# Performance work log

Hardware: AMD Instinct MI355X
Metric: run time of the kernel (lower is better)

## Reference

```python
import jax, jax.numpy as jnp
import numpy as np

B, S, IN, D, H, L, M = 8, 1024, 256, 512, 8, 2, 64
DK = D // H
FF = 4 * D
EPS = 1e-5


def setup_inputs() -> dict:
    key = jax.random.key(0)
    ks = jax.random.split(key, 16)
    w = lambda k, shape: jax.random.normal(k, shape, jnp.float32) * 0.02
    return {
        "inputs": jax.random.normal(ks[0], (B, S, IN), jnp.float32),
        "lengths": jax.random.randint(ks[1], (B,), S // 2, S + 1),
        "W_in": w(ks[2], (IN, D)), "b_in": jnp.zeros((D,), jnp.float32),
        # per-layer stacked params (leading axis L) for lax.scan
        "Wq": w(ks[3], (L, D, D)), "bq": jnp.zeros((L, D), jnp.float32),
        "Wk": w(ks[4], (L, D, D)), "bk": jnp.zeros((L, D), jnp.float32),
        "Wv": w(ks[5], (L, D, D)), "bv": jnp.zeros((L, D), jnp.float32),
        "Wo": w(ks[6], (L, D, D)), "bo": jnp.zeros((L, D), jnp.float32),
        "rel_bias": w(ks[7], (L, H, 2 * M - 1)),
        "W1": w(ks[8], (L, D, FF)), "b1": jnp.zeros((L, FF), jnp.float32),
        "W2": w(ks[9], (L, FF, D)), "b2": jnp.zeros((L, D), jnp.float32),
        "g1": jnp.ones((L, D), jnp.float32), "be1": jnp.zeros((L, D), jnp.float32),
        "g2": jnp.ones((L, D), jnp.float32), "be2": jnp.zeros((L, D), jnp.float32),
        "gf": jnp.ones((D,), jnp.float32), "bef": jnp.zeros((D,), jnp.float32),
    }


def _ln(x, g, b):
    m = jnp.mean(x, axis=-1, keepdims=True)
    v = jnp.mean(jnp.square(x - m), axis=-1, keepdims=True)
    return (x - m) * jax.lax.rsqrt(v + EPS) * g + b


def _sinusoid_pe(seq_len, d_model):
    pos = jnp.arange(seq_len, dtype=jnp.float32)[:, None]
    div = jnp.exp(jnp.arange(0, d_model, 2, dtype=jnp.float32) * (-np.log(10000.0) / d_model))
    pe = jnp.zeros((seq_len, d_model), jnp.float32)
    pe = pe.at[:, 0::2].set(jnp.sin(pos * div))
    pe = pe.at[:, 1::2].set(jnp.cos(pos * div))
    return pe


def _encoder(inputs, lengths, W_in, b_in, Wq, bq, Wk, bk, Wv, bv, Wo, bo,
             rel_bias, W1, b1, W2, b2, g1, be1, g2, be2, gf, bef):
    x = inputs @ W_in + b_in                      # (B,S,D)
    x = x + _sinusoid_pe(S, D)[None]
    pad = jnp.arange(S)[None, :] >= lengths[:, None]   # (B,S) True = padded key

    r = jnp.arange(S)
    rel_idx = jnp.clip(r[:, None] - r[None, :], -(M - 1), M - 1) + (M - 1)  # (S,S)
    scale = 1.0 / np.sqrt(DK)

    def layer(x, p):
        (wq, bq_, wk, bk_, wv, bv_, wo, bo_, rb, w1, b1_, w2, b2_, g1_, be1_, g2_, be2_) = p
        # --- self-attention sublayer (pre-norm) ---
        h = _ln(x, g1_, be1_)
        q = (h @ wq + bq_).reshape(B, S, H, DK).transpose(0, 2, 1, 3)  # (B,H,S,DK)
        k = (h @ wk + bk_).reshape(B, S, H, DK).transpose(0, 2, 1, 3)
        v = (h @ wv + bv_).reshape(B, S, H, DK).transpose(0, 2, 1, 3)
        scores = jnp.einsum('bhqd,bhkd->bhqk', q, k) * scale
        scores = scores + rb[:, rel_idx][None]            # (H,S,S) relative bias
        scores = jnp.where(pad[:, None, None, :], -jnp.inf, scores)
        attn = jax.nn.softmax(scores, axis=-1)
        o = jnp.einsum('bhqk,bhkd->bhqd', attn, v)
        o = o.transpose(0, 2, 1, 3).reshape(B, S, D) @ wo + bo_
        x = x + o
        # --- FFN sublayer (pre-norm) ---
        h = _ln(x, g2_, be2_)
        x = x + (jax.nn.relu(h @ w1 + b1_) @ w2 + b2_)
        return x, None

    stacked = (Wq, bq, Wk, bk, Wv, bv, Wo, bo, rel_bias, W1, b1, W2, b2, g1, be1, g2, be2)
    x, _ = jax.lax.scan(layer, x, stacked)
    return _ln(x, gf, bef)


def reference(inputs, lengths, W_in, b_in, Wq, bq, Wk, bk, Wv, bv, Wo, bo,
              rel_bias, W1, b1, W2, b2, g1, be1, g2, be2, gf, bef):
    return _encoder(inputs, lengths, W_in, b_in, Wq, bq, Wk, bk, Wv, bv, Wo, bo,
                    rel_bias, W1, b1, W2, b2, g1, be1, g2, be2, gf, bef)
```

## Files before the change

kernel.cpp:

```cpp
#include <hip/hip_runtime.h>
#include <hip/hip_bf16.h>

typedef unsigned short u16;
typedef unsigned int u32;
typedef __bf16 v8bf __attribute__((ext_vector_type(8)));
typedef float v4f __attribute__((ext_vector_type(4)));

#define B_SZ 8
#define S_LEN 1024
#define IN_DIM 256
#define DMODEL 512
#define NHEAD 8
#define DK 64
#define FF_DIM 2048
#define MROWS (B_SZ * S_LEN)
#define QSCALE 0.1803368801111204f

__device__ __forceinline__ u16 f2bf(float f) {
    unsigned int x = __float_as_uint(f);
    unsigned int r = (x + 0x7fffu + ((x >> 16) & 1u)) >> 16;
    return (u16)r;
}

__device__ __forceinline__ void gl16(const u16* g, u16* l) {
    __builtin_amdgcn_global_load_lds((const __attribute__((address_space(1))) unsigned int*)g,
                                     (__attribute__((address_space(3))) unsigned int*)l, 16, 0, 0);
}

__global__ __launch_bounds__(256) void conv_bf16_kernel(const float* __restrict__ in,
                                                        u16* __restrict__ out, int n4) {
    int i = blockIdx.x * 256 + threadIdx.x;
    if (i < n4) {
        float4 v = ((const float4*)in)[i];
        ushort4 o;
        o.x = f2bf(v.x); o.y = f2bf(v.y); o.z = f2bf(v.z); o.w = f2bf(v.w);
        ((ushort4*)out)[i] = o;
    }
}

struct TDesc { const float* src; u16* dst; int K; int N; };
struct TArgs { TDesc d[13]; };

__global__ void transpose_conv_kernel(TArgs args) {
    TDesc t = args.d[blockIdx.z];
    int k0 = blockIdx.x * 32, n0 = blockIdx.y * 32;
    if (k0 >= t.K || n0 >= t.N) return;
    __shared__ float tile[32][33];
    int tx = threadIdx.x, ty = threadIdx.y;
#pragma unroll
    for (int j = 0; j < 4; j++) {
        int k = k0 + ty + j * 8;
        tile[ty + j * 8][tx] = t.src[(size_t)k * t.N + n0 + tx];
    }
    __syncthreads();
#pragma unroll
    for (int j = 0; j < 4; j++) {
        int n = n0 + ty + j * 8;
        t.dst[(size_t)n * t.K + k0 + tx] = f2bf(tile[tx][ty + j * 8]);
    }
}

template <bool OUT_BF16>
__global__ __launch_bounds__(256) void ln_kernel(const float* __restrict__ x,
                                                 const float* __restrict__ g,
                                                 const float* __restrict__ b,
                                                 void* __restrict__ out) {
    int row = blockIdx.x * 4 + (threadIdx.x >> 6);
    int lane = threadIdx.x & 63;
    const float4* xr = (const float4*)(x + (size_t)row * DMODEL);
    float4 v0 = xr[lane], v1 = xr[lane + 64];
    float s = v0.x + v0.y + v0.z + v0.w + v1.x + v1.y + v1.z + v1.w;
    float sq = v0.x * v0.x + v0.y * v0.y + v0.z * v0.z + v0.w * v0.w +
               v1.x * v1.x + v1.y * v1.y + v1.z * v1.z + v1.w * v1.w;
#pragma unroll
    for (int m = 1; m < 64; m <<= 1) {
        s += __shfl_xor(s, m);
        sq += __shfl_xor(sq, m);
    }
    float mean = s * (1.0f / DMODEL);
    float var = sq * (1.0f / DMODEL) - mean * mean;
    float rstd = rsqrtf(var + 1e-5f);
    const float4* g4 = (const float4*)g;
    const float4* b4 = (const float4*)b;
    float4 ga = g4[lane], gb = g4[lane + 64], ba = b4[lane], bb = b4[lane + 64];
    float4 r0, r1;
    r0.x = (v0.x - mean) * rstd * ga.x + ba.x;
    r0.y = (v0.y - mean) * rstd * ga.y + ba.y;
    r0.z = (v0.z - mean) * rstd * ga.z + ba.z;
    r0.w = (v0.w - mean) * rstd * ga.w + ba.w;
    r1.x = (v1.x - mean) * rstd * gb.x + bb.x;
    r1.y = (v1.y - mean) * rstd * gb.y + bb.y;
    r1.z = (v1.z - mean) * rstd * gb.z + bb.z;
    r1.w = (v1.w - mean) * rstd * gb.w + bb.w;
    if (OUT_BF16) {
        ushort4 o0, o1;
        o0.x = f2bf(r0.x); o0.y = f2bf(r0.y); o0.z = f2bf(r0.z); o0.w = f2bf(r0.w);
        o1.x = f2bf(r1.x); o1.y = f2bf(r1.y); o1.z = f2bf(r1.z); o1.w = f2bf(r1.w);
        ((ushort4*)out)[(size_t)row * 128 + lane] = o0;
        ((ushort4*)out)[(size_t)row * 128 + 64 + lane] = o1;
    } else {
        ((float4*)out)[(size_t)row * 128 + lane] = r0;
        ((float4*)out)[(size_t)row * 128 + 64 + lane] = r1;
    }
}

template <int MT, int NT>
__device__ __forceinline__ void gemm_core(const u16* __restrict__ A, const u16* __restrict__ Bt,
                                          int K, v4f (&acc)[MT][NT]) {
    constexpr int BM = MT * 32;
    constexpr int BN = NT * 32;
    __shared__ u16 As[BM * 64];
    __shared__ u16 Bs[BN * 64];
    int tid = threadIdx.x;
    int n0 = blockIdx.x * BN, m0 = blockIdx.y * BM;
    int w = tid >> 6, lane = tid & 63;
    int wr = (w >> 1) * (BM / 2), wc = (w & 1) * (BN / 2);
    int lr = lane & 15, lq = lane >> 4;
    int r8 = lane >> 3, cb = lane & 7;
    int scol = (cb ^ r8) * 8;

    v4f zero = {0.f, 0.f, 0.f, 0.f};
#pragma unroll
    for (int i = 0; i < MT; i++)
#pragma unroll
        for (int j = 0; j < NT; j++) acc[i][j] = zero;

    const u16* gA[MT]; u16* lA[MT];
#pragma unroll
    for (int j = 0; j < MT; j++) {
        int row0 = (MT * 8) * w + j * 8;
        gA[j] = A + (size_t)(m0 + row0 + r8) * K + scol;
        lA[j] = As + row0 * 64;
    }
    const u16* gB[NT]; u16* lB[NT];
#pragma unroll
    for (int j = 0; j < NT; j++) {
        int row0 = (NT * 8) * w + j * 8;
        gB[j] = Bt + (size_t)(n0 + row0 + r8) * K + scol;
        lB[j] = Bs + row0 * 64;
    }

    for (int k0 = 0; k0 < K; k0 += 64) {
#pragma unroll
        for (int j = 0; j < MT; j++) gl16(gA[j], lA[j]);
#pragma unroll
        for (int j = 0; j < NT; j++) gl16(gB[j], lB[j]);
        __syncthreads();
#pragma unroll
        for (int kk = 0; kk < 2; kk++) {
            int xb = ((kk * 4 + lq) ^ (lr & 7)) * 8;
            v8bf af[MT], bfr[NT];
#pragma unroll
            for (int i = 0; i < MT; i++)
                af[i] = *(const v8bf*)&As[(wr + i * 16 + lr) * 64 + xb];
#pragma unroll
            for (int j = 0; j < NT; j++)
                bfr[j] = *(const v8bf*)&Bs[(wc + j * 16 + lr) * 64 + xb];
#pragma unroll
            for (int mt = 0; mt < MT; mt++)
#pragma unroll
                for (int nt = 0; nt < NT; nt++)
                    acc[mt][nt] = __builtin_amdgcn_mfma_f32_16x16x32_bf16(af[mt], bfr[nt], acc[mt][nt], 0, 0, 0);
        }
        __syncthreads();
#pragma unroll
        for (int j = 0; j < MT; j++) gA[j] += 64;
#pragma unroll
        for (int j = 0; j < NT; j++) gB[j] += 64;
    }
}

__global__ __launch_bounds__(256) void gemm_in_kernel(const u16* __restrict__ A,
                                                      const u16* __restrict__ Bt,
                                                      const float* __restrict__ bias,
                                                      float* __restrict__ Out, int K) {
    v4f acc[4][2];
    gemm_core<4, 2>(A, Bt, K, acc);
    int tid = threadIdx.x, w = tid >> 6, lane = tid & 63;
    int lr = lane & 15, lq = lane >> 4;
    int wr = (w >> 1) * 64, wc = (w & 1) * 32;
    int n0 = blockIdx.x * 64, m0 = blockIdx.y * 128;
#pragma unroll
    for (int mt = 0; mt < 4; mt++) {
#pragma unroll
        for (int nt = 0; nt < 2; nt++) {
            int col = n0 + wc + nt * 16 + lr;
            float bcol = bias[col];
            float freq = __builtin_amdgcn_exp2f((float)(col & ~1) * (-0.025953277f));
#pragma unroll
            for (int reg = 0; reg < 4; reg++) {
                int row = m0 + wr + mt * 16 + lq * 4 + reg;
                float rev = (float)(row & (S_LEN - 1)) * freq * 0.15915494309189535f;
                float fr = __builtin_amdgcn_fractf(rev);
                float pe = (col & 1) ? __builtin_amdgcn_cosf(fr) : __builtin_amdgcn_sinf(fr);
                Out[(size_t)row * DMODEL + col] = acc[mt][nt][reg] + bcol + pe;
            }
        }
    }
}

__global__ __launch_bounds__(256) void gemm_qkv_kernel(const u16* __restrict__ A,
                                                       const u16* __restrict__ Bt,
                                                       const float* __restrict__ bq,
                                                       const float* __restrict__ bk,
                                                       const float* __restrict__ bv,
                                                       u16* __restrict__ Qo,
                                                       u16* __restrict__ Ko,
                                                       u16* __restrict__ Vto, int K) {
    v4f acc[4][4];
    gemm_core<4, 4>(A, Bt, K, acc);
    int tid = threadIdx.x, w = tid >> 6, lane = tid & 63;
    int lr = lane & 15, lq = lane >> 4;
    int wr = (w >> 1) * 64, wc = (w & 1) * 64;
    int n0 = blockIdx.x * 128, m0 = blockIdx.y * 128;
    int seg = n0 >> 9;
#pragma unroll
    for (int mt = 0; mt < 4; mt++) {
#pragma unroll
        for (int nt = 0; nt < 4; nt++) {
            int col = (n0 + wc + nt * 16 + lr) & (DMODEL - 1);
            if (seg == 0) {
                float bcol = bq[col];
#pragma unroll
                for (int reg = 0; reg < 4; reg++) {
                    int row = m0 + wr + mt * 16 + lq * 4 + reg;
                    Qo[(size_t)row * DMODEL + col] = f2bf((acc[mt][nt][reg] + bcol) * QSCALE);
                }
            } else if (seg == 1) {
                float bcol = bk[col];
#pragma unroll
                for (int reg = 0; reg < 4; reg++) {
                    int row = m0 + wr + mt * 16 + lq * 4 + reg;
                    Ko[(size_t)row * DMODEL + col] = f2bf(acc[mt][nt][reg] + bcol);
                }
            } else {
                float bcol = bv[col];
                int row0 = m0 + wr + mt * 16 + lq * 4;
                int bb = row0 >> 10, s0 = row0 & (S_LEN - 1);
                ushort4 o;
                o.x = f2bf(acc[mt][nt][0] + bcol);
                o.y = f2bf(acc[mt][nt][1] + bcol);
                o.z = f2bf(acc[mt][nt][2] + bcol);
                o.w = f2bf(acc[mt][nt][3] + bcol);
                *(ushort4*)(Vto + ((size_t)(bb * DMODEL + col)) * S_LEN + s0) = o;
            }
        }
    }
}

__global__ __launch_bounds__(256) void gemm_relu_kernel(const u16* __restrict__ A,
                                                        const u16* __restrict__ Bt,
                                                        const float* __restrict__ bias,
                                                        u16* __restrict__ Out, int N, int K) {
    v4f acc[4][4];
    gemm_core<4, 4>(A, Bt, K, acc);
    int tid = threadIdx.x, w = tid >> 6, lane = tid & 63;
    int lr = lane & 15, lq = lane >> 4;
    int wr = (w >> 1) * 64, wc = (w & 1) * 64;
    int n0 = blockIdx.x * 128, m0 = blockIdx.y * 128;
#pragma unroll
    for (int mt = 0; mt < 4; mt++) {
#pragma unroll
        for (int nt = 0; nt < 4; nt++) {
            int col = n0 + wc + nt * 16 + lr;
            float bcol = bias[col];
#pragma unroll
            for (int reg = 0; reg < 4; reg++) {
                int row = m0 + wr + mt * 16 + lq * 4 + reg;
                Out[(size_t)row * N + col] = f2bf(fmaxf(acc[mt][nt][reg] + bcol, 0.0f));
            }
        }
    }
}

__global__ __launch_bounds__(256) void gemm_res_kernel(const u16* __restrict__ A,
                                                       const u16* __restrict__ Bt,
                                                       const float* __restrict__ bias,
                                                       float* __restrict__ Out, int K) {
    v4f acc[4][2];
    gemm_core<4, 2>(A, Bt, K, acc);
    int tid = threadIdx.x, w = tid >> 6, lane = tid & 63;
    int lr = lane & 15, lq = lane >> 4;
    int wr = (w >> 1) * 64, wc = (w & 1) * 32;
    int n0 = blockIdx.x * 64, m0 = blockIdx.y * 128;
#pragma unroll
    for (int mt = 0; mt < 4; mt++) {
#pragma unroll
        for (int nt = 0; nt < 2; nt++) {
            int col = n0 + wc + nt * 16 + lr;
            float bcol = bias[col];
#pragma unroll
            for (int reg = 0; reg < 4; reg++) {
                int row = m0 + wr + mt * 16 + lq * 4 + reg;
                size_t idx = (size_t)row * DMODEL + col;
                Out[idx] = Out[idx] + acc[mt][nt][reg] + bcol;
            }
        }
    }
}

__global__ __launch_bounds__(256, 4) void fattn_kernel(const u16* __restrict__ Qg,
                                                       const u16* __restrict__ Kg,
                                                       const u16* __restrict__ Vtg,
                                                       const float* __restrict__ rb,
                                                       const int* __restrict__ lengths,
                                                       u16* __restrict__ Op,
                                                       float* __restrict__ lsums) {
    int bid = blockIdx.x;
    int wg = (bid & 7) * 128 + (bid >> 3);
    int i = wg & 127;
    int h = wg >> 7;
    int b = i & 7;
    int qt = (i >> 3) & 7;
    int kvh = (i >> 6) & 1;
    int tid = threadIdx.x, w = tid >> 6, lane = tid & 63;
    int lr = lane & 15, lq = lane >> 4;
    __shared__ u16 Ks[2][64 * 64];
    __shared__ u16 Vs[2][64 * 64];
    __shared__ float rbs[128];
    int len = lengths[b];
    if (tid < 127) rbs[tid] = rb[h * 127 + tid] * 1.4426950408889634f;

    int l2 = ((len + 127) >> 7) << 6;
    int kstart = kvh ? l2 : 0;
    int kend = kvh ? len : l2;

    int qw = qt * 128 + w * 32;
    v8bf qa[2][2];
#pragma unroll
    for (int ntq = 0; ntq < 2; ntq++) {
        size_t qrow = ((size_t)(b * S_LEN + qw + ntq * 16 + lr)) * DMODEL + h * DK;
        qa[ntq][0] = *(const v8bf*)(Qg + qrow + lq * 8);
        qa[ntq][1] = *(const v8bf*)(Qg + qrow + 32 + lq * 8);
    }

    v4f zero = {0.f, 0.f, 0.f, 0.f};
    v4f Oacc[4][2];
#pragma unroll
    for (int dt = 0; dt < 4; dt++)
#pragma unroll
        for (int nt = 0; nt < 2; nt++) Oacc[dt][nt] = zero;
    float lsum[2] = {0.f, 0.f};

    const u16* Kbase = Kg + ((size_t)b * S_LEN) * DMODEL + h * DK;
    const u16* Vbase = Vtg + ((size_t)(b * DMODEL + h * DK)) * S_LEN;
    int r8 = lane >> 3, cb = lane & 7;
    int swz = (cb ^ r8) * 8;

#pragma unroll
    for (int j = 0; j < 2; j++) {
        int row0 = w * 16 + j * 8;
        gl16(Kbase + (size_t)(kstart + row0 + r8) * DMODEL + swz, Ks[0] + row0 * 64);
        gl16(Vbase + (size_t)(row0 + r8) * S_LEN + kstart + swz, Vs[0] + row0 * 64);
    }

    int pb = 0;
    for (int kb0 = kstart; kb0 < kend; kb0 += 64, pb ^= 1) {
        __syncthreads();
        __builtin_amdgcn_sched_barrier(0);

        int nxt = kb0 + 64;
        if (nxt < kend) {
#pragma unroll
            for (int j = 0; j < 2; j++) {
                int row0 = w * 16 + j * 8;
                gl16(Kbase + (size_t)(nxt + row0 + r8) * DMODEL + swz, Ks[pb ^ 1] + row0 * 64);
                gl16(Vbase + (size_t)(row0 + r8) * S_LEN + nxt + swz, Vs[pb ^ 1] + row0 * 64);
            }
        }
        const u16* Ksc = Ks[pb];
        const u16* Vsc = Vs[pb];

        v4f S[4][2];
        __builtin_amdgcn_s_setprio(1);
#pragma unroll
        for (int mtk = 0; mtk < 4; mtk++) {
            int xb0 = (lq ^ (lr & 7)) * 8;
            int xb1 = ((4 + lq) ^ (lr & 7)) * 8;
            v8bf kf0 = *(const v8bf*)&Ksc[(mtk * 16 + lr) * 64 + xb0];
            v8bf kf1 = *(const v8bf*)&Ksc[(mtk * 16 + lr) * 64 + xb1];
#pragma unroll
            for (int ntq = 0; ntq < 2; ntq++) {
                v4f s = __builtin_amdgcn_mfma_f32_16x16x32_bf16(kf0, qa[ntq][0], zero, 0, 0, 0);
                S[mtk][ntq] = __builtin_amdgcn_mfma_f32_16x16x32_bf16(kf1, qa[ntq][1], s, 0, 0, 0);
            }
        }
        __builtin_amdgcn_s_setprio(0);

        bool edge = (kb0 + 64 > len);
        int dmin = qw - (kb0 + 63), dmax = qw + 31 - kb0;
        bool perel = !(dmax <= -63 || dmin >= 63);
        float bconst = (dmax <= -63) ? rbs[0] : rbs[126];
        uint2 pks[4][2];
#pragma unroll
        for (int mtk = 0; mtk < 4; mtk++) {
#pragma unroll
            for (int ntq = 0; ntq < 2; ntq++) {
                int q = qw + ntq * 16 + lr;
                float p[4];
#pragma unroll
                for (int r = 0; r < 4; r++) {
                    int key = kb0 + mtk * 16 + lq * 4 + r;
                    float s = S[mtk][ntq][r];
                    if (perel) {
                        int d = q - key;
                        d = d < -63 ? -63 : (d > 63 ? 63 : d);
                        s += rbs[d + 63];
                    } else {
                        s += bconst;
                    }
                    float pv = __builtin_amdgcn_exp2f(s);
                    if (edge && key >= len) pv = 0.f;
                    lsum[ntq] += pv;
                    p[r] = pv;
                }
                pks[mtk][ntq].x = (__float_as_uint(p[1]) & 0xffff0000u) | (__float_as_uint(p[0]) >> 16);
                pks[mtk][ntq].y = (__float_as_uint(p[3]) & 0xffff0000u) | (__float_as_uint(p[2]) >> 16);
            }
        }

        __builtin_amdgcn_s_setprio(1);
#pragma unroll
        for (int kh = 0; kh < 2; kh++) {
            uint4 tp0 = {pks[kh * 2][0].x, pks[kh * 2][0].y, pks[kh * 2 + 1][0].x, pks[kh * 2 + 1][0].y};
            uint4 tp1 = {pks[kh * 2][1].x, pks[kh * 2][1].y, pks[kh * 2 + 1][1].x, pks[kh * 2 + 1][1].y};
            v8bf pb0 = *(v8bf*)&tp0;
            v8bf pb1 = *(v8bf*)&tp1;
            int gl = kh * 4 + (lq >> 1);
            int sub = (lq & 1) * 4;
#pragma unroll
            for (int dt = 0; dt < 4; dt++) {
                int drow = (dt * 16 + lr) * 64;
                uint2 lo = *(const uint2*)&Vsc[drow + ((gl ^ (lr & 7)) * 8 + sub)];
                uint2 hi = *(const uint2*)&Vsc[drow + (((gl + 2) ^ (lr & 7)) * 8 + sub)];
                uint4 tv = {lo.x, lo.y, hi.x, hi.y};
                v8bf va = *(v8bf*)&tv;
                Oacc[dt][0] = __builtin_amdgcn_mfma_f32_16x16x32_bf16(va, pb0, Oacc[dt][0], 0, 0, 0);
                Oacc[dt][1] = __builtin_amdgcn_mfma_f32_16x16x32_bf16(va, pb1, Oacc[dt][1], 0, 0, 0);
            }
        }
        __builtin_amdgcn_s_setprio(0);
    }

    float lsumR[2];
#pragma unroll
    for (int ntq = 0; ntq < 2; ntq++) {
        float s = lsum[ntq];
        s += __shfl_xor(s, 16);
        s += __shfl_xor(s, 32);
        lsumR[ntq] = s;
    }
    if (lq == 0) {
#pragma unroll
        for (int ntq = 0; ntq < 2; ntq++) {
            int q = qw + ntq * 16 + lr;
            lsums[((size_t)kvh * MROWS + b * S_LEN + q) * NHEAD + h] = lsumR[ntq];
        }
    }
    u16* Oh = Op + (size_t)kvh * MROWS * DMODEL;
#pragma unroll
    for (int dt = 0; dt < 4; dt++) {
#pragma unroll
        for (int ntq = 0; ntq < 2; ntq++) {
            size_t off = (size_t)(b * S_LEN + qw + ntq * 16 + lr) * DMODEL + h * DK + dt * 16 + lq * 4;
            ushort4 o;
            o.x = f2bf(Oacc[dt][ntq][0]);
            o.y = f2bf(Oacc[dt][ntq][1]);
            o.z = f2bf(Oacc[dt][ntq][2]);
            o.w = f2bf(Oacc[dt][ntq][3]);
            *(ushort4*)(Oh + off) = o;
        }
    }
}

__device__ __forceinline__ u32 comb2(u32 a, u32 b, float inv) {
    float r0 = (__uint_as_float(a << 16) + __uint_as_float(b << 16)) * inv;
    float r1 = (__uint_as_float(a & 0xffff0000u) + __uint_as_float(b & 0xffff0000u)) * inv;
    return (u32)f2bf(r0) | ((u32)f2bf(r1) << 16);
}

__global__ __launch_bounds__(256) void attn_combine_kernel(const u16* __restrict__ Op,
                                                           const float* __restrict__ lsums,
                                                           u16* __restrict__ out) {
    int row = blockIdx.x * 4 + (threadIdx.x >> 6);
    int lane = threadIdx.x & 63;
    int h = lane >> 3;
    float l0 = lsums[(size_t)row * NHEAD + h];
    float l1 = lsums[((size_t)MROWS + row) * NHEAD + h];
    float inv = 1.0f / (l0 + l1);
    size_t base = (size_t)row * DMODEL + lane * 8;
    uint4 a = *(const uint4*)(Op + base);
    uint4 c = *(const uint4*)(Op + (size_t)MROWS * DMODEL + base);
    uint4 o;
    o.x = comb2(a.x, c.x, inv);
    o.y = comb2(a.y, c.y, inv);
    o.z = comb2(a.z, c.z, inv);
    o.w = comb2(a.w, c.w, inv);
    *(uint4*)(out + base) = o;
}

extern "C" void kernel_launch(void* const* d_in, const int* in_sizes, int n_in,
                              void* d_out, int out_size, void* d_ws, size_t ws_size,
                              hipStream_t stream) {
    const float* inputs   = (const float*)d_in[0];
    const int*   lengths  = (const int*)d_in[1];
    const float* W_in     = (const float*)d_in[2];
    const float* b_in     = (const float*)d_in[3];
    const float* Wq       = (const float*)d_in[4];
    const float* bq       = (const float*)d_in[5];
    const float* Wk       = (const float*)d_in[6];
    const float* bk       = (const float*)d_in[7];
    const float* Wv       = (const float*)d_in[8];
    const float* bv       = (const float*)d_in[9];
    const float* Wo       = (const float*)d_in[10];
    const float* bo       = (const float*)d_in[11];
    const float* rel_bias = (const float*)d_in[12];
    const float* W1       = (const float*)d_in[13];
    const float* b1       = (const float*)d_in[14];
    const float* W2       = (const float*)d_in[15];
    const float* b2       = (const float*)d_in[16];
    const float* g1       = (const float*)d_in[17];
    const float* be1      = (const float*)d_in[18];
    const float* g2       = (const float*)d_in[19];
    const float* be2      = (const float*)d_in[20];
    const float* gf       = (const float*)d_in[21];
    const float* bef      = (const float*)d_in[22];

    char* ws = (char*)d_ws;
    float* xbuf = (float*)ws;          ws += (size_t)MROWS * DMODEL * 4;
    u16* hbuf   = (u16*)ws;            ws += (size_t)MROWS * DMODEL * 2;
    u16* aobuf  = hbuf;
    u16* qbf    = (u16*)ws;            ws += (size_t)MROWS * FF_DIM * 2;
    u16* kbf    = qbf + (size_t)MROWS * DMODEL;
    u16* vtbf   = kbf + (size_t)MROWS * DMODEL;
    float* lsums = (float*)(vtbf + (size_t)MROWS * DMODEL);
    u16* tbuf   = qbf;
    u16* inbf   = qbf;
    u16* opart  = (u16*)d_out;
    u16* wt_in  = (u16*)ws;            ws += (size_t)DMODEL * IN_DIM * 2;
    u16 *qkvw[2], *wto[2], *wt1[2], *wt2[2];
    for (int l = 0; l < 2; l++) { qkvw[l] = (u16*)ws; ws += (size_t)3 * DMODEL * DMODEL * 2; }
    for (int l = 0; l < 2; l++) { wto[l] = (u16*)ws; ws += (size_t)DMODEL * DMODEL * 2; }
    for (int l = 0; l < 2; l++) { wt1[l] = (u16*)ws; ws += (size_t)FF_DIM * DMODEL * 2; }
    for (int l = 0; l < 2; l++) { wt2[l] = (u16*)ws; ws += (size_t)DMODEL * FF_DIM * 2; }

    TArgs ta;
    int ti = 0;
    ta.d[ti++] = {W_in, wt_in, IN_DIM, DMODEL};
    for (int l = 0; l < 2; l++) {
        ta.d[ti++] = {Wq + (size_t)l * DMODEL * DMODEL, qkvw[l], DMODEL, DMODEL};
        ta.d[ti++] = {Wk + (size_t)l * DMODEL * DMODEL, qkvw[l] + (size_t)DMODEL * DMODEL, DMODEL, DMODEL};
        ta.d[ti++] = {Wv + (size_t)l * DMODEL * DMODEL, qkvw[l] + (size_t)2 * DMODEL * DMODEL, DMODEL, DMODEL};
        ta.d[ti++] = {Wo + (size_t)l * DMODEL * DMODEL, wto[l], DMODEL, DMODEL};
        ta.d[ti++] = {W1 + (size_t)l * DMODEL * FF_DIM, wt1[l], DMODEL, FF_DIM};
        ta.d[ti++] = {W2 + (size_t)l * FF_DIM * DMODEL, wt2[l], FF_DIM, DMODEL};
    }

    conv_bf16_kernel<<<dim3((MROWS * IN_DIM / 4 + 255) / 256), 256, 0, stream>>>(
        inputs, inbf, MROWS * IN_DIM / 4);
    transpose_conv_kernel<<<dim3(64, 64, 13), dim3(32, 8), 0, stream>>>(ta);

    gemm_in_kernel<<<dim3(DMODEL / 64, MROWS / 128), 256, 0, stream>>>(
        inbf, wt_in, b_in, xbuf, IN_DIM);

    for (int l = 0; l < 2; l++) {
        ln_kernel<true><<<MROWS / 4, 256, 0, stream>>>(xbuf, g1 + l * DMODEL, be1 + l * DMODEL, hbuf);
        gemm_qkv_kernel<<<dim3(3 * DMODEL / 128, MROWS / 128), 256, 0, stream>>>(
            hbuf, qkvw[l], bq + l * DMODEL, bk + l * DMODEL, bv + l * DMODEL,
            qbf, kbf, vtbf, DMODEL);
        fattn_kernel<<<dim3(1024), 256, 0, stream>>>(
            qbf, kbf, vtbf, rel_bias + (size_t)l * NHEAD * 127, lengths, opart, lsums);
        attn_combine_kernel<<<MROWS / 4, 256, 0, stream>>>(opart, lsums, aobuf);
        gemm_res_kernel<<<dim3(DMODEL / 64, MROWS / 128), 256, 0, stream>>>(
            aobuf, wto[l], bo + l * DMODEL, xbuf, DMODEL);
        ln_kernel<true><<<MROWS / 4, 256, 0, stream>>>(xbuf, g2 + l * DMODEL, be2 + l * DMODEL, hbuf);
        gemm_relu_kernel<<<dim3(FF_DIM / 128, MROWS / 128), 256, 0, stream>>>(
            hbuf, wt1[l], b1 + l * FF_DIM, tbuf, FF_DIM, DMODEL);
        gemm_res_kernel<<<dim3(DMODEL / 64, MROWS / 128), 256, 0, stream>>>(
            tbuf, wt2[l], b2 + l * DMODEL, xbuf, FF_DIM);
    }
    ln_kernel<false><<<MROWS / 4, 256, 0, stream>>>(xbuf, gf, bef, d_out);
}
```

Before: 467.2 us.

## Triple-buffer K/V tiles in flash attention with explicit vmcnt waits

Replaces the double-buffered K/V shared-memory pipeline in the attention kernel with a three-stage ring buffer. Two chunks are prefetched up front, and each iteration waits with s_waitcnt vmcnt on only the older loads before a raw s_barrier, so a load has two iterations of compute to hide behind. Shared memory per block grows from 32KB to 48KB, which may reduce occupancy under launch_bounds(256,4). The hand-counted vmcnt values depend on how many loads gl16 issues. The prologue also loads a second chunk even when there is only one.

```diff
diff --git a/kernel.cpp b/kernel.cpp
--- a/kernel.cpp
+++ b/kernel.cpp
@@ -315,8 +315,8 @@
     int kvh = (i >> 6) & 1;
     int tid = threadIdx.x, w = tid >> 6, lane = tid & 63;
     int lr = lane & 15, lq = lane >> 4;
-    __shared__ u16 Ks[2][64 * 64];
-    __shared__ u16 Vs[2][64 * 64];
+    __shared__ u16 Ks[3][64 * 64];
+    __shared__ u16 Vs[3][64 * 64];
     __shared__ float rbs[128];
     int len = lengths[b];
     if (tid < 127) rbs[tid] = rb[h * 127 + tid] * 1.4426950408889634f;
@@ -324,6 +324,7 @@
     int l2 = ((len + 127) >> 7) << 6;
     int kstart = kvh ? l2 : 0;
     int kend = kvh ? len : l2;
+    int nchunks = (kend - kstart + 63) >> 6;
 
     int qw = qt * 128 + w * 32;
     v8bf qa[2][2];
@@ -353,23 +354,37 @@
         gl16(Kbase + (size_t)(kstart + row0 + r8) * DMODEL + swz, Ks[0] + row0 * 64);
         gl16(Vbase + (size_t)(row0 + r8) * S_LEN + kstart + swz, Vs[0] + row0 * 64);
     }
-
-    int pb = 0;
-    for (int kb0 = kstart; kb0 < kend; kb0 += 64, pb ^= 1) {
-        __syncthreads();
-        __builtin_amdgcn_sched_barrier(0);
-
-        int nxt = kb0 + 64;
-        if (nxt < kend) {
+#pragma unroll
+    for (int j = 0; j < 2; j++) {
+        int row0 = w * 16 + j * 8;
+        gl16(Kbase + (size_t)(kstart + 64 + row0 + r8) * DMODEL + swz, Ks[1] + row0 * 64);
+        gl16(Vbase + (size_t)(row0 + r8) * S_LEN + kstart + 64 + swz, Vs[1] + row0 * 64);
+    }
+    __syncthreads();
+
+    u16 *KsA = Ks[0], *VsA = Vs[0];
+    u16 *KsB = Ks[1], *VsB = Vs[1];
+    u16 *KsC = Ks[2], *VsC = Vs[2];
+
+    for (int ci = 0; ci < nchunks; ci++) {
+        int kb0 = kstart + ci * 64;
+        if (ci > 0) {
+            if (ci + 1 < nchunks) asm volatile("s_waitcnt vmcnt(4)" ::: "memory");
+            else                  asm volatile("s_waitcnt vmcnt(0)" ::: "memory");
+            __builtin_amdgcn_s_barrier();
+            __builtin_amdgcn_sched_barrier(0);
+        }
+        if (ci + 2 < nchunks) {
+            int nk = kb0 + 128;
 #pragma unroll
             for (int j = 0; j < 2; j++) {
                 int row0 = w * 16 + j * 8;
-                gl16(Kbase + (size_t)(nxt + row0 + r8) * DMODEL + swz, Ks[pb ^ 1] + row0 * 64);
-                gl16(Vbase + (size_t)(row0 + r8) * S_LEN + nxt + swz, Vs[pb ^ 1] + row0 * 64);
-            }
-        }
-        const u16* Ksc = Ks[pb];
-        const u16* Vsc = Vs[pb];
+                gl16(Kbase + (size_t)(nk + row0 + r8) * DMODEL + swz, KsC + row0 * 64);
+                gl16(Vbase + (size_t)(row0 + r8) * S_LEN + nk + swz, VsC + row0 * 64);
+            }
+        }
+        const u16* Ksc = KsA;
+        const u16* Vsc = VsA;
 
         v4f S[4][2];
         __builtin_amdgcn_s_setprio(1);
@@ -440,6 +455,10 @@
             }
         }
         __builtin_amdgcn_s_setprio(0);
+
+        u16* t;
+        t = KsA; KsA = KsB; KsB = KsC; KsC = t;
+        t = VsA; VsA = VsB; VsB = VsC; VsC = t;
     }
 
     float lsumR[2];
```

Result: no change. 468.3 us (+0.2%).
